# Kernel tuning notes

Hardware: AMD Instinct MI355X
Metric: run time of the kernel (lower is better)

## Reference

```python
import jax, jax.numpy as jnp
import numpy as np

T, D, O, E, R = 16384, 4096, 4096, 8, 64  # tokens, in_feat, out_feat, n_adapters, max_rank


def setup_inputs() -> dict:
    key = jax.random.key(0)
    ks = jax.random.split(key, 6)
    x = jax.random.normal(ks[0], (T, D), jnp.float32)
    base_output = jax.random.normal(ks[1], (T, O), jnp.float32)
    A = jax.random.normal(ks[2], (E, D, R), jnp.float32) * 0.02  # loraA per adapter
    B = jax.random.normal(ks[3], (E, R, O), jnp.float32) * 0.02  # loraB per adapter
    scaling = jax.random.uniform(ks[4], (E,), jnp.float32, 0.5, 2.0)  # lora_alpha/rank per adapter
    adapter_ids = jax.random.randint(ks[5], (T,), 0, E, dtype=jnp.int32)  # per-token routing
    return {"x": x, "base_output": base_output, "A": A, "B": B,
            "scaling": scaling, "adapter_ids": adapter_ids}


def reference(x, base_output, A, B, scaling, adapter_ids):
    """S-LoRA batched multi-adapter forward: out = base + (x @ A_i) @ B_i * s_i,
    with adapter i routed per token. Expressed as E masked low-rank GEMMs
    (loop over the small fixed adapter set, vectorized over tokens)."""
    out = base_output
    for e in range(E):
        gate = (adapter_ids == e).astype(x.dtype) * scaling[e]  # (T,)
        h = x @ A[e]                                            # (T, R)
        out = out + (h @ B[e]) * gate[:, None]                  # (T, O)
    return out
```

## Files before the change

### kernel.cpp

```cpp
#include <hip/hip_runtime.h>

#define TT 16384
#define DD 4096
#define OO 4096
#define NE 8
#define RRK 64
#define KSPLIT 8
#define KCHUNK 512

typedef _Float16 f16x8 __attribute__((ext_vector_type(8)));
typedef _Float16 f16x4 __attribute__((ext_vector_type(4)));
typedef float f32x4 __attribute__((ext_vector_type(4)));

#define CNT_OFF 0
#define PERM_OFF 1024
#define AT_OFF (1u << 20)
#define BT_OFF (5u << 20)
#define HP_OFF (9u << 20)
#define H_OFF (41u << 20)

__global__ void prep_kernel(const int* __restrict__ ids,
                            const float* __restrict__ A,
                            const float* __restrict__ B,
                            int* __restrict__ cnt,
                            int* __restrict__ perm,
                            _Float16* __restrict__ At,
                            _Float16* __restrict__ Bt) {
  const int bid = blockIdx.x, tid = threadIdx.x;
  if (bid < 64) {
    int t = bid * 256 + tid;
    int e = ids[t];
    int pos = atomicAdd(&cnt[e], 1);
    perm[e * TT + pos] = t;
    return;
  }
  __shared__ float tile[64][65];
  if (bid < 576) {
    int idx = bid - 64;
    int e = idx >> 6, kb = (idx & 63) << 6;
    #pragma unroll
    for (int i = 0; i < 16; ++i) {
      int lin = i * 256 + tid;
      int kr = lin >> 6, r = lin & 63;
      tile[kr][r] = A[((size_t)e * DD + kb + kr) * RRK + r];
    }
    __syncthreads();
    #pragma unroll
    for (int i = 0; i < 16; ++i) {
      int lin = i * 256 + tid;
      int r = lin >> 6, kk = lin & 63;
      At[((size_t)e * RRK + r) * DD + kb + kk] = (_Float16)tile[kk][r];
    }
  } else {
    int idx = bid - 576;
    int e = idx >> 6, ob = (idx & 63) << 6;
    #pragma unroll
    for (int i = 0; i < 16; ++i) {
      int lin = i * 256 + tid;
      int r = lin >> 6, o = lin & 63;
      tile[r][o] = B[((size_t)e * RRK + r) * OO + ob + o];
    }
    __syncthreads();
    #pragma unroll
    for (int i = 0; i < 16; ++i) {
      int lin = i * 256 + tid;
      int o = lin >> 6, r2 = lin & 63;
      Bt[((size_t)e * OO + ob + o) * RRK + r2] = (_Float16)tile[r2][o];
    }
  }
}

__global__ __launch_bounds__(256, 4)
void lora_stage1(const float* __restrict__ x,
                 const _Float16* __restrict__ At,
                 const int* __restrict__ cnt,
                 const int* __restrict__ perm,
                 float* __restrict__ HP) {
  const int tid = threadIdx.x;
  const int lane = tid & 63, w = tid >> 6;
  const int lr = lane & 15;
  const int kq = (lane >> 4) << 3;

  int tiles = 0;
  #pragma unroll
  for (int ee = 0; ee < NE; ++ee) tiles += (cnt[ee] + 63) >> 6;

  for (int wi = blockIdx.x; wi < tiles * KSPLIT; wi += gridDim.x) {
    int tile = wi >> 3, s = wi & 7;
    int e = 0, base = 0, n_e = 0;
    {
      int acc0 = 0;
      #pragma unroll
      for (int ee = 0; ee < NE; ++ee) {
        int c = cnt[ee];
        int tl = (c + 63) >> 6;
        if (tile >= acc0 && tile < acc0 + tl) { e = ee; base = acc0; n_e = c; }
        acc0 += tl;
      }
    }
    int m0 = (tile - base) << 6;
    int kbase = s * KCHUNK;

    int arow = m0 + w * 16 + lr;
    int atok = perm[e * TT + (arow < n_e ? arow : n_e - 1)];
    const float* xp = x + (size_t)atok * DD + kbase + kq;
    const _Float16* ap = At + (size_t)e * RRK * DD + kbase + kq;

    f32x4 acc[4] = {};

    for (int k0 = 0; k0 < KCHUNK; k0 += 64) {
      f16x8 xa[2];
      #pragma unroll
      for (int ks = 0; ks < 2; ++ks) {
        float4 u0 = *(const float4*)(xp + k0 + ks * 32);
        float4 u1 = *(const float4*)(xp + k0 + ks * 32 + 4);
        f16x8 v;
        v[0] = (_Float16)u0.x; v[1] = (_Float16)u0.y;
        v[2] = (_Float16)u0.z; v[3] = (_Float16)u0.w;
        v[4] = (_Float16)u1.x; v[5] = (_Float16)u1.y;
        v[6] = (_Float16)u1.z; v[7] = (_Float16)u1.w;
        xa[ks] = v;
      }
      #pragma unroll
      for (int ks = 0; ks < 2; ++ks) {
        #pragma unroll
        for (int nf = 0; nf < 4; ++nf) {
          f16x8 bfr = *(const f16x8*)(ap + (size_t)(nf * 16 + lr) * DD + k0 + ks * 32);
          acc[nf] = __builtin_amdgcn_mfma_f32_16x16x32_f16(xa[ks], bfr, acc[nf], 0, 0, 0);
        }
      }
    }

    const int rq = (lane >> 4) << 2;
    #pragma unroll
    for (int rg = 0; rg < 4; ++rg) {
      int row = m0 + w * 16 + rq + rg;
      if (row < n_e) {
        int tk = perm[e * TT + row];
        float* hp = HP + ((size_t)s * TT + tk) * RRK + lr;
        #pragma unroll
        for (int nf = 0; nf < 4; ++nf) hp[nf * 16] = acc[nf][rg];
      }
    }
  }
}

__global__ void lora_reduce(const float* __restrict__ HP,
                            const float* __restrict__ scaling,
                            const int* __restrict__ ids,
                            _Float16* __restrict__ H) {
  int i = blockIdx.x * 256 + threadIdx.x;
  int t = i >> 4;
  int rg = (i & 15) << 2;
  float s = scaling[ids[t]];
  f32x4 sum = {};
  #pragma unroll
  for (int sp = 0; sp < KSPLIT; ++sp) {
    sum += *(const f32x4*)(HP + ((size_t)sp * TT + t) * RRK + rg);
  }
  f16x4 h;
  #pragma unroll
  for (int j = 0; j < 4; ++j) h[j] = (_Float16)(sum[j] * s);
  *(f16x4*)(H + (size_t)t * RRK + rg) = h;
}

__global__ __launch_bounds__(256, 4)
void lora_stage2(const float* __restrict__ baseo,
                 const _Float16* __restrict__ Bt,
                 const _Float16* __restrict__ H,
                 const int* __restrict__ cnt,
                 const int* __restrict__ perm,
                 float* __restrict__ out) {
  const int tid = threadIdx.x;
  const int lane = tid & 63, w = tid >> 6;
  const int lr = lane & 15;
  const int kq = (lane >> 4) << 3;
  const int g4 = (lane >> 4) << 2;

  int tot = 0;
  #pragma unroll
  for (int ee = 0; ee < NE; ++ee) tot += ((cnt[ee] + 63) >> 6) << 4;

  for (int wi = blockIdx.x; wi < tot; wi += gridDim.x) {
    int e = 0, base = 0, n_e = 0;
    {
      int acc0 = 0;
      #pragma unroll
      for (int ee = 0; ee < NE; ++ee) {
        int c = cnt[ee];
        int tl = ((c + 63) >> 6) << 4;
        if (wi >= acc0 && wi < acc0 + tl) { e = ee; base = acc0; n_e = c; }
        acc0 += tl;
      }
    }
    int local = wi - base;
    int tiles_m = (n_e + 63) >> 6;
    int mt = local % tiles_m;
    int nt = local / tiles_m;
    int m0 = mt << 6, o0 = nt << 8;

    int row = m0 + w * 16 + lr;
    bool valid = row < n_e;
    int tk = perm[e * TT + (valid ? row : n_e - 1)];

    const _Float16* hp = H + (size_t)tk * RRK + kq;
    f16x8 hf0 = *(const f16x8*)(hp);
    f16x8 hf1 = *(const f16x8*)(hp + 32);

    const _Float16* bp = Bt + ((size_t)e * OO + o0 + lr) * RRK + kq;

    f32x4 acc[16];
    #pragma unroll
    for (int of = 0; of < 16; ++of) acc[of] = (f32x4){0.f, 0.f, 0.f, 0.f};

    #pragma unroll
    for (int of = 0; of < 16; ++of) {
      f16x8 b0 = *(const f16x8*)(bp + (size_t)of * 16 * RRK);
      f16x8 b1 = *(const f16x8*)(bp + (size_t)of * 16 * RRK + 32);
      acc[of] = __builtin_amdgcn_mfma_f32_16x16x32_f16(b0, hf0, acc[of], 0, 0, 0);
      acc[of] = __builtin_amdgcn_mfma_f32_16x16x32_f16(b1, hf1, acc[of], 0, 0, 0);
    }

    if (valid) {
      size_t rowoff = (size_t)tk * OO + o0 + g4;
      #pragma unroll
      for (int of = 0; of < 16; ++of) {
        size_t off = rowoff + of * 16;
        float4 b4 = *(const float4*)(baseo + off);
        float4 r4;
        r4.x = b4.x + acc[of][0];
        r4.y = b4.y + acc[of][1];
        r4.z = b4.z + acc[of][2];
        r4.w = b4.w + acc[of][3];
        *(float4*)(out + off) = r4;
      }
    }
  }
}

extern "C" void kernel_launch(void* const* d_in, const int* in_sizes, int n_in,
                              void* d_out, int out_size, void* d_ws, size_t ws_size,
                              hipStream_t stream) {
  const float* x = (const float*)d_in[0];
  const float* baseo = (const float*)d_in[1];
  const float* A = (const float*)d_in[2];
  const float* B = (const float*)d_in[3];
  const float* scaling = (const float*)d_in[4];
  const int* ids = (const int*)d_in[5];
  float* out = (float*)d_out;
  char* ws = (char*)d_ws;

  int* cnt = (int*)(ws + CNT_OFF);
  int* perm = (int*)(ws + PERM_OFF);
  _Float16* At = (_Float16*)(ws + AT_OFF);
  _Float16* Bt = (_Float16*)(ws + BT_OFF);
  float* HP = (float*)(ws + HP_OFF);
  _Float16* H = (_Float16*)(ws + H_OFF);

  hipMemsetAsync(cnt, 0, NE * sizeof(int), stream);
  hipLaunchKernelGGL(prep_kernel, dim3(1088), dim3(256), 0, stream,
                     ids, A, B, cnt, perm, At, Bt);
  hipLaunchKernelGGL(lora_stage1, dim3(2048), dim3(256), 0, stream,
                     x, At, cnt, perm, HP);
  hipLaunchKernelGGL(lora_reduce, dim3(1024), dim3(256), 0, stream,
                     HP, scaling, ids, H);
  hipLaunchKernelGGL(lora_stage2, dim3(4096), dim3(256), 0, stream,
                     baseo, Bt, H, cnt, perm, out);
}
```

Baseline: 349.8 us.

## Widen per-block tiles in both LoRA stages to reuse adapter fragments

Stage 1 now handles two 64-row token tiles per work item and shares each loaded At fragment between them, halving A-matrix reads per token. Stage 2 keeps a 128-column Bt panel in registers and loops over up to four token tiles, software-prefetching the next H row. Launch bounds drop to 3 waves per SIMD and grid sizes shrink to match the smaller work count. The trade is higher register pressure and lower occupancy in exchange for less redundant loading of the adapter weights; the dominant base_output/out traffic is unchanged.

```diff
diff --git a/kernel.cpp b/kernel.cpp
--- a/kernel.cpp
+++ b/kernel.cpp
@@ -70,7 +70,7 @@
   }
 }
 
-__global__ __launch_bounds__(256, 4)
+__global__ __launch_bounds__(256, 3)
 void lora_stage1(const float* __restrict__ x,
                  const _Float16* __restrict__ At,
                  const int* __restrict__ cnt,
@@ -81,52 +81,74 @@
   const int lr = lane & 15;
   const int kq = (lane >> 4) << 3;
 
-  int tiles = 0;
+  int tot = 0;
   #pragma unroll
-  for (int ee = 0; ee < NE; ++ee) tiles += (cnt[ee] + 63) >> 6;
-
-  for (int wi = blockIdx.x; wi < tiles * KSPLIT; wi += gridDim.x) {
-    int tile = wi >> 3, s = wi & 7;
+  for (int ee = 0; ee < NE; ++ee) {
+    int tl = (cnt[ee] + 63) >> 6;
+    tot += ((tl + 1) >> 1) * KSPLIT;
+  }
+
+  for (int wi = blockIdx.x; wi < tot; wi += gridDim.x) {
     int e = 0, base = 0, n_e = 0;
     {
       int acc0 = 0;
       #pragma unroll
       for (int ee = 0; ee < NE; ++ee) {
         int c = cnt[ee];
-        int tl = (c + 63) >> 6;
-        if (tile >= acc0 && tile < acc0 + tl) { e = ee; base = acc0; n_e = c; }
-        acc0 += tl;
-      }
-    }
-    int m0 = (tile - base) << 6;
+        int work = ((((c + 63) >> 6) + 1) >> 1) * KSPLIT;
+        if (wi >= acc0 && wi < acc0 + work) { e = ee; base = acc0; n_e = c; }
+        acc0 += work;
+      }
+    }
+    int local = wi - base;
+    int s = local & (KSPLIT - 1);
+    int ch = local >> 3;
     int kbase = s * KCHUNK;
-
-    int arow = m0 + w * 16 + lr;
-    int atok = perm[e * TT + (arow < n_e ? arow : n_e - 1)];
-    const float* xp = x + (size_t)atok * DD + kbase + kq;
+    int m0 = ch << 7;
+
+    const int prow = e * TT;
+    int arow0 = m0 + w * 16 + lr;
+    int arow1 = arow0 + 64;
+    int atok0 = perm[prow + (arow0 < n_e ? arow0 : n_e - 1)];
+    int atok1 = perm[prow + (arow1 < n_e ? arow1 : n_e - 1)];
+    const float* xp0 = x + (size_t)atok0 * DD + kbase + kq;
+    const float* xp1 = x + (size_t)atok1 * DD + kbase + kq;
     const _Float16* ap = At + (size_t)e * RRK * DD + kbase + kq;
 
-    f32x4 acc[4] = {};
+    f32x4 acc0[4] = {};
+    f32x4 acc1[4] = {};
 
     for (int k0 = 0; k0 < KCHUNK; k0 += 64) {
-      f16x8 xa[2];
+      float4 u00 = *(const float4*)(xp0 + k0);
+      float4 u01 = *(const float4*)(xp0 + k0 + 4);
+      float4 u02 = *(const float4*)(xp0 + k0 + 32);
+      float4 u03 = *(const float4*)(xp0 + k0 + 36);
+      float4 u10 = *(const float4*)(xp1 + k0);
+      float4 u11 = *(const float4*)(xp1 + k0 + 4);
+      float4 u12 = *(const float4*)(xp1 + k0 + 32);
+      float4 u13 = *(const float4*)(xp1 + k0 + 36);
+      f16x8 at[4][2];
+      #pragma unroll
+      for (int nf = 0; nf < 4; ++nf) {
+        #pragma unroll
+        for (int ks = 0; ks < 2; ++ks)
+          at[nf][ks] = *(const f16x8*)(ap + (size_t)(nf * 16 + lr) * DD + k0 + ks * 32);
+      }
+      f16x8 xa0[2], xa1[2];
+      xa0[0][0]=(_Float16)u00.x; xa0[0][1]=(_Float16)u00.y; xa0[0][2]=(_Float16)u00.z; xa0[0][3]=(_Float16)u00.w;
+      xa0[0][4]=(_Float16)u01.x; xa0[0][5]=(_Float16)u01.y; xa0[0][6]=(_Float16)u01.z; xa0[0][7]=(_Float16)u01.w;
+      xa0[1][0]=(_Float16)u02.x; xa0[1][1]=(_Float16)u02.y; xa0[1][2]=(_Float16)u02.z; xa0[1][3]=(_Float16)u02.w;
+      xa0[1][4]=(_Float16)u03.x; xa0[1][5]=(_Float16)u03.y; xa0[1][6]=(_Float16)u03.z; xa0[1][7]=(_Float16)u03.w;
+      xa1[0][0]=(_Float16)u10.x; xa1[0][1]=(_Float16)u10.y; xa1[0][2]=(_Float16)u10.z; xa1[0][3]=(_Float16)u10.w;
+      xa1[0][4]=(_Float16)u11.x; xa1[0][5]=(_Float16)u11.y; xa1[0][6]=(_Float16)u11.z; xa1[0][7]=(_Float16)u11.w;
+      xa1[1][0]=(_Float16)u12.x; xa1[1][1]=(_Float16)u12.y; xa1[1][2]=(_Float16)u12.z; xa1[1][3]=(_Float16)u12.w;
+      xa1[1][4]=(_Float16)u13.x; xa1[1][5]=(_Float16)u13.y; xa1[1][6]=(_Float16)u13.z; xa1[1][7]=(_Float16)u13.w;
       #pragma unroll
       for (int ks = 0; ks < 2; ++ks) {
-        float4 u0 = *(const float4*)(xp + k0 + ks * 32);
-        float4 u1 = *(const float4*)(xp + k0 + ks * 32 + 4);
-        f16x8 v;
-        v[0] = (_Float16)u0.x; v[1] = (_Float16)u0.y;
-        v[2] = (_Float16)u0.z; v[3] = (_Float16)u0.w;
-        v[4] = (_Float16)u1.x; v[5] = (_Float16)u1.y;
-        v[6] = (_Float16)u1.z; v[7] = (_Float16)u1.w;
-        xa[ks] = v;
-      }
-      #pragma unroll
-      for (int ks = 0; ks < 2; ++ks) {
         #pragma unroll
         for (int nf = 0; nf < 4; ++nf) {
-          f16x8 bfr = *(const f16x8*)(ap + (size_t)(nf * 16 + lr) * DD + k0 + ks * 32);
-          acc[nf] = __builtin_amdgcn_mfma_f32_16x16x32_f16(xa[ks], bfr, acc[nf], 0, 0, 0);
+          acc0[nf] = __builtin_amdgcn_mfma_f32_16x16x32_f16(xa0[ks], at[nf][ks], acc0[nf], 0, 0, 0);
+          acc1[nf] = __builtin_amdgcn_mfma_f32_16x16x32_f16(xa1[ks], at[nf][ks], acc1[nf], 0, 0, 0);
         }
       }
     }
@@ -134,12 +156,19 @@
     const int rq = (lane >> 4) << 2;
     #pragma unroll
     for (int rg = 0; rg < 4; ++rg) {
-      int row = m0 + w * 16 + rq + rg;
-      if (row < n_e) {
-        int tk = perm[e * TT + row];
+      int row0 = m0 + w * 16 + rq + rg;
+      if (row0 < n_e) {
+        int tk = perm[prow + row0];
         float* hp = HP + ((size_t)s * TT + tk) * RRK + lr;
         #pragma unroll
-        for (int nf = 0; nf < 4; ++nf) hp[nf * 16] = acc[nf][rg];
+        for (int nf = 0; nf < 4; ++nf) hp[nf * 16] = acc0[nf][rg];
+      }
+      int row1 = row0 + 64;
+      if (row1 < n_e) {
+        int tk = perm[prow + row1];
+        float* hp = HP + ((size_t)s * TT + tk) * RRK + lr;
+        #pragma unroll
+        for (int nf = 0; nf < 4; ++nf) hp[nf * 16] = acc1[nf][rg];
       }
     }
   }
@@ -164,7 +193,7 @@
   *(f16x4*)(H + (size_t)t * RRK + rg) = h;
 }
 
-__global__ __launch_bounds__(256, 4)
+__global__ __launch_bounds__(256, 3)
 void lora_stage2(const float* __restrict__ baseo,
                  const _Float16* __restrict__ Bt,
                  const _Float16* __restrict__ H,
@@ -179,7 +208,10 @@
 
   int tot = 0;
   #pragma unroll
-  for (int ee = 0; ee < NE; ++ee) tot += ((cnt[ee] + 63) >> 6) << 4;
+  for (int ee = 0; ee < NE; ++ee) {
+    int tl = (cnt[ee] + 63) >> 6;
+    tot += ((tl + 3) >> 2) << 5;
+  }
 
   for (int wi = blockIdx.x; wi < tot; wi += gridDim.x) {
     int e = 0, base = 0, n_e = 0;
@@ -188,52 +220,72 @@
       #pragma unroll
       for (int ee = 0; ee < NE; ++ee) {
         int c = cnt[ee];
-        int tl = ((c + 63) >> 6) << 4;
-        if (wi >= acc0 && wi < acc0 + tl) { e = ee; base = acc0; n_e = c; }
-        acc0 += tl;
+        int work = ((((c + 63) >> 6) + 3) >> 2) << 5;
+        if (wi >= acc0 && wi < acc0 + work) { e = ee; base = acc0; n_e = c; }
+        acc0 += work;
       }
     }
     int local = wi - base;
+    int panel = local & 31;
+    int ch = local >> 5;
+    int o0 = panel << 7;
+    int tbase = ch << 2;
     int tiles_m = (n_e + 63) >> 6;
-    int mt = local % tiles_m;
-    int nt = local / tiles_m;
-    int m0 = mt << 6, o0 = nt << 8;
-
-    int row = m0 + w * 16 + lr;
-    bool valid = row < n_e;
-    int tk = perm[e * TT + (valid ? row : n_e - 1)];
-
-    const _Float16* hp = H + (size_t)tk * RRK + kq;
-    f16x8 hf0 = *(const f16x8*)(hp);
-    f16x8 hf1 = *(const f16x8*)(hp + 32);
-
-    const _Float16* bp = Bt + ((size_t)e * OO + o0 + lr) * RRK + kq;
-
-    f32x4 acc[16];
-    #pragma unroll
-    for (int of = 0; of < 16; ++of) acc[of] = (f32x4){0.f, 0.f, 0.f, 0.f};
-
-    #pragma unroll
-    for (int of = 0; of < 16; ++of) {
-      f16x8 b0 = *(const f16x8*)(bp + (size_t)of * 16 * RRK);
-      f16x8 b1 = *(const f16x8*)(bp + (size_t)of * 16 * RRK + 32);
-      acc[of] = __builtin_amdgcn_mfma_f32_16x16x32_f16(b0, hf0, acc[of], 0, 0, 0);
-      acc[of] = __builtin_amdgcn_mfma_f32_16x16x32_f16(b1, hf1, acc[of], 0, 0, 0);
-    }
-
-    if (valid) {
-      size_t rowoff = (size_t)tk * OO + o0 + g4;
-      #pragma unroll
-      for (int of = 0; of < 16; ++of) {
-        size_t off = rowoff + of * 16;
-        float4 b4 = *(const float4*)(baseo + off);
-        float4 r4;
-        r4.x = b4.x + acc[of][0];
-        r4.y = b4.y + acc[of][1];
-        r4.z = b4.z + acc[of][2];
-        r4.w = b4.w + acc[of][3];
-        *(float4*)(out + off) = r4;
-      }
+    int ntile = tiles_m - tbase;
+    if (ntile > 4) ntile = 4;
+
+    f16x8 bf0[8], bf1[8];
+    {
+      const _Float16* bp = Bt + ((size_t)e * OO + o0 + lr) * RRK + kq;
+      #pragma unroll
+      for (int of = 0; of < 8; ++of) {
+        bf0[of] = *(const f16x8*)(bp + (size_t)of * 16 * RRK);
+        bf1[of] = *(const f16x8*)(bp + (size_t)of * 16 * RRK + 32);
+      }
+    }
+
+    const int prow = e * TT;
+    int row_c = tbase * 64 + w * 16 + lr;
+    bool v_c = row_c < n_e;
+    int tk_c = perm[prow + (v_c ? row_c : n_e - 1)];
+    f16x8 hf0_c = *(const f16x8*)(H + (size_t)tk_c * RRK + kq);
+    f16x8 hf1_c = *(const f16x8*)(H + (size_t)tk_c * RRK + kq + 32);
+
+    for (int m = 0; m < ntile; ++m) {
+      int row_n = row_c + 64;
+      bool v_n = false; int tk_n = tk_c;
+      f16x8 hf0_n = hf0_c, hf1_n = hf1_c;
+      if (m + 1 < ntile) {
+        v_n = row_n < n_e;
+        tk_n = perm[prow + (v_n ? row_n : n_e - 1)];
+        hf0_n = *(const f16x8*)(H + (size_t)tk_n * RRK + kq);
+        hf1_n = *(const f16x8*)(H + (size_t)tk_n * RRK + kq + 32);
+      }
+
+      f32x4 acc[8];
+      #pragma unroll
+      for (int of = 0; of < 8; ++of) acc[of] = (f32x4){0.f, 0.f, 0.f, 0.f};
+      #pragma unroll
+      for (int of = 0; of < 8; ++of) {
+        acc[of] = __builtin_amdgcn_mfma_f32_16x16x32_f16(bf0[of], hf0_c, acc[of], 0, 0, 0);
+        acc[of] = __builtin_amdgcn_mfma_f32_16x16x32_f16(bf1[of], hf1_c, acc[of], 0, 0, 0);
+      }
+
+      if (v_c) {
+        size_t rowoff = (size_t)tk_c * OO + o0 + g4;
+        #pragma unroll
+        for (int of = 0; of < 8; ++of) {
+          size_t off2 = rowoff + (size_t)of * 16;
+          float4 b4 = *(const float4*)(baseo + off2);
+          float4 r4;
+          r4.x = b4.x + acc[of][0];
+          r4.y = b4.y + acc[of][1];
+          r4.z = b4.z + acc[of][2];
+          r4.w = b4.w + acc[of][3];
+          *(float4*)(out + off2) = r4;
+        }
+      }
+      row_c = row_n; v_c = v_n; tk_c = tk_n; hf0_c = hf0_n; hf1_c = hf1_n;
     }
   }
 }
@@ -260,10 +312,10 @@
   hipMemsetAsync(cnt, 0, NE * sizeof(int), stream);
   hipLaunchKernelGGL(prep_kernel, dim3(1088), dim3(256), 0, stream,
                      ids, A, B, cnt, perm, At, Bt);
-  hipLaunchKernelGGL(lora_stage1, dim3(2048), dim3(256), 0, stream,
+  hipLaunchKernelGGL(lora_stage1, dim3(1088), dim3(256), 0, stream,
                      x, At, cnt, perm, HP);
   hipLaunchKernelGGL(lora_reduce, dim3(1024), dim3(256), 0, stream,
                      HP, scaling, ids, H);
-  hipLaunchKernelGGL(lora_stage2, dim3(4096), dim3(256), 0, stream,
+  hipLaunchKernelGGL(lora_stage2, dim3(2048), dim3(256), 0, stream,
                      baseo, Bt, H, cnt, perm, out);
 }
```

After: 351.9 us. No clear change (+0.6%).
